# Optimization experiments

Measured on AMD Instinct MI355X. Metric: run time of the kernel, lower is better.

The kernel has to match this reference:

```python
import jax, jax.numpy as jnp
import numpy as np

NM = 50000   # member nodes
NP = 50000   # provider nodes
DM = 96      # member feature dim
DP = 128     # provider feature dim
IN_DIM = 128
HID = 256
LAT = 64
E = 1000000


def _sage_conv(x, src, dst, n, Wl, Wr, b):
    # PyG SAGEConv, mean aggregation: out = lin_l(mean_j x_j) + lin_r(x)
    msg = x[src]                                           # [E2, F]
    agg = jax.ops.segment_sum(msg, dst, num_segments=n)    # [N, F]
    deg = jax.ops.segment_sum(jnp.ones(src.shape[0], x.dtype), dst, num_segments=n)
    agg = agg / jnp.maximum(deg, 1.0)[:, None]
    return agg @ Wl.T + b + x @ Wr.T


def setup_inputs() -> dict:
    key = jax.random.key(0)
    ks = jax.random.split(key, 12)
    def g(k, shape, scale):
        return jax.random.normal(k, shape, jnp.float32) * scale
    inp = {
        "x_member": jax.random.normal(ks[0], (NM, DM), jnp.float32),
        "x_provider": jax.random.normal(ks[1], (NP, DP), jnp.float32),
        "edge_index": jnp.stack([
            jax.random.randint(ks[2], (E,), 0, NP),   # provider idx
            jax.random.randint(ks[3], (E,), 0, NM),   # member idx
        ], axis=0),
        # SAGEConv 1
        "W1l": g(ks[4], (HID, IN_DIM), (1.0 / IN_DIM) ** 0.5),
        "W1r": g(ks[5], (HID, IN_DIM), (1.0 / IN_DIM) ** 0.5),
        "b1": jnp.zeros((HID,), jnp.float32),
        # SAGEConv 2
        "W2l": g(ks[6], (LAT, HID), (1.0 / HID) ** 0.5),
        "W2r": g(ks[7], (LAT, HID), (1.0 / HID) ** 0.5),
        "b2": jnp.zeros((LAT,), jnp.float32),
        # decoder Linear(latent, in_dim)
        "Wd": g(ks[8], (IN_DIM, LAT), (1.0 / LAT) ** 0.5),
        "bd": jnp.zeros((IN_DIM,), jnp.float32),
    }
    return inp


def reference(x_member, x_provider, edge_index, W1l, W1r, b1, W2l, W2r, b2, Wd, bd):
    # pad member features to max_dim and concat (members first)
    xm = jnp.pad(x_member, ((0, 0), (0, IN_DIM - DM)))
    x = jnp.concatenate([xm, x_provider], axis=0)          # [NM+NP, IN_DIM]

    provider_idx = edge_index[0]
    member_idx = edge_index[1]
    # faithful to source: member indices are offset by NM in the combined graph
    src = jnp.concatenate([provider_idx, member_idx + NM])
    dst = jnp.concatenate([member_idx + NM, provider_idx])
    n = NM + NP

    h = jax.nn.relu(_sage_conv(x, src, dst, n, W1l, W1r, b1))
    # dropout: eval mode -> identity
    z = _sage_conv(h, src, dst, n, W2l, W2r, b2)            # [N, LAT]
    x_hat = z @ Wd.T + bd                                   # [N, IN_DIM]

    x_hat_member = x_hat[:NM]
    x_hat_provider = x_hat[NM:]
    member_z = z[:NM]
    provider_z = z[NM:]
    edge_logits = jnp.sum(provider_z[provider_idx] * member_z[member_idx], axis=1)
    return (x_hat_member, x_hat_provider, edge_logits)
```

## Files before the change

kernel.cpp:

```cpp
#include <hip/hip_runtime.h>
#include <stdint.h>

#define NMEM 50000
#define NTOT 100000
#define DMEM 96
#define DPRV 128
#define IND  128
#define HID  256
#define LATD 64
#define NEDGE 1000000

#define NB   196
#define VSH  9
#define NBV  512
#define EPB  4096

#define PREP_PCOUNT 245
#define PREP_CANON  418
#define G3B 1563

typedef __bf16 v8bf  __attribute__((ext_vector_type(8)));
typedef float  f32x4 __attribute__((ext_vector_type(4)));

__device__ __forceinline__ float bf2f(uint32_t u) {
    union { uint32_t u; float f; } x; x.u = u << 16; return x.f;
}
__device__ __forceinline__ uint32_t f2bf(float f) {
    union { float f; uint32_t u; } x; x.f = f;
    uint32_t r = x.u + 0x7fffu + ((x.u >> 16) & 1u);
    return r >> 16;
}
__device__ __forceinline__ int ld_ei(const int* ei, int idx, int i64) {
    return i64 ? ei[2 * idx] : ei[idx];
}

__global__ void k_detect(const uint16_t* __restrict__ w1l, const int* __restrict__ ei,
                         int* __restrict__ flags) {
    __shared__ int c1, c2;
    if (threadIdx.x == 0) { c1 = 0; c2 = 0; }
    __syncthreads();
    int big = 0;
    for (int i = threadIdx.x; i < 32768; i += 256) {
        float w = bf2f(w1l[i]);
        if (!(w > -2.0f && w < 2.0f)) big++;
    }
    int zhi = 0;
    for (int j = threadIdx.x; j < 2048; j += 256)
        if (ei[2 * j + 1] == 0) zhi++;
    atomicAdd(&c1, big);
    atomicAdd(&c2, zhi);
    __syncthreads();
    if (threadIdx.x == 0) {
        flags[0] = (c1 > 64) ? 1 : 0;
        flags[1] = (c2 > 1024) ? 1 : 0;
    }
}

__global__ __launch_bounds__(256) void k_prep(const void* w1l, const void* w1r,
                                              const void* w2l, const void* w2r,
                                              const void* wd, const void* b1,
                                              const void* b2, const void* bd,
                                              const void* xm, const void* xp,
                                              const int* __restrict__ ei,
                                              uint16_t* __restrict__ dstw,
                                              float* __restrict__ dstb,
                                              uint16_t* __restrict__ Px,
                                              uint16_t* __restrict__ Rx,
                                              int* __restrict__ bcount,
                                              const int* __restrict__ flags) {
    __shared__ int h[NB];
    int bid = blockIdx.x;
    int t = threadIdx.x;
    int f32in = flags[0];
    if (bid < PREP_PCOUNT) {
        for (int i = t; i < NB; i += 256) h[i] = 0;
        __syncthreads();
        int i64 = flags[1];
        int j0 = bid * EPB;
        int jend = min(j0 + EPB, NEDGE);
        for (int j = j0 + t; j < jend; j += 256) {
            int p = ld_ei(ei, j, i64), m = ld_ei(ei, NEDGE + j, i64);
            atomicAdd(&h[(NMEM + m) >> VSH], 1);
            atomicAdd(&h[p >> VSH], 1);
        }
        __syncthreads();
        for (int i = t; i < NB; i += 256) atomicAdd(&bcount[i], h[i]);
        return;
    }
    if (bid < PREP_PCOUNT + PREP_CANON) {
        int g = (bid - PREP_PCOUNT) * 256 + t;
        if (g < 106496) {
            const void* src; int off;
            if (g < 65536) { int n = g >> 8, k = g & 255;
                src = (k < 128) ? w1l : w1r; off = n * 128 + (k & 127); }
            else if (g < 81920) { src = w2l; off = g - 65536; }
            else if (g < 98304) { src = w2r; off = g - 81920; }
            else                { src = wd;  off = g - 98304; }
            dstw[g] = f32in ? (uint16_t)f2bf(((const float*)src)[off])
                            : ((const uint16_t*)src)[off];
        } else if (g < 106944) {
            int o = g - 106496;
            const void* src; int off;
            if (o < 256)      { src = b1; off = o; }
            else if (o < 320) { src = b2; off = o - 256; }
            else              { src = bd; off = o - 320; }
            dstb[o] = f32in ? ((const float*)src)[off] : bf2f(((const uint16_t*)src)[off]);
        }
        return;
    }
    int idx = (bid - PREP_PCOUNT - PREP_CANON) * 256 + t;
    if (idx >= NTOT * 16) return;
    int v = idx >> 4, dblk = idx & 15;
    int d0 = dblk * 8;
    union { uint4 q; uint16_t u[8]; } o;
    if (v < NMEM) {
        if (d0 < DMEM) {
            if (f32in) {
                const float* s = (const float*)xm + (size_t)v * DMEM + d0;
                uint4 lo = *(const uint4*)s;
                uint4 hi = *(const uint4*)(s + 4);
                const float* lf = (const float*)&lo;
                const float* hf = (const float*)&hi;
#pragma unroll
                for (int i = 0; i < 4; i++) o.u[i] = (uint16_t)f2bf(lf[i]);
#pragma unroll
                for (int i = 0; i < 4; i++) o.u[4 + i] = (uint16_t)f2bf(hf[i]);
            } else {
                o.q = *(const uint4*)((const uint16_t*)xm + (size_t)v * DMEM + d0);
            }
        } else {
            o.q = (uint4){0, 0, 0, 0};
        }
    } else {
        int vv = v - NMEM;
        if (f32in) {
            const float* s = (const float*)xp + (size_t)vv * DPRV + d0;
            uint4 lo = *(const uint4*)s;
            uint4 hi = *(const uint4*)(s + 4);
            const float* lf = (const float*)&lo;
            const float* hf = (const float*)&hi;
#pragma unroll
            for (int i = 0; i < 4; i++) o.u[i] = (uint16_t)f2bf(lf[i]);
#pragma unroll
            for (int i = 0; i < 4; i++) o.u[4 + i] = (uint16_t)f2bf(hf[i]);
        } else {
            o.q = *(const uint4*)((const uint16_t*)xp + (size_t)vv * DPRV + d0);
        }
    }
    if (d0 < 64) *(uint4*)(Px + (size_t)v * 64 + d0) = o.q;
    else         *(uint4*)(Rx + (size_t)v * 64 + (d0 - 64)) = o.q;
}

__global__ void k_bscan(const int* __restrict__ bcount, int* __restrict__ bbase,
                        int* __restrict__ bcursor, int* __restrict__ row_start) {
    __shared__ int s[256];
    int t = threadIdx.x;
    int v = (t < NB) ? bcount[t] : 0;
    s[t] = v; __syncthreads();
    for (int off = 1; off < 256; off <<= 1) {
        int x = (t >= off) ? s[t - off] : 0;
        __syncthreads();
        s[t] += x;
        __syncthreads();
    }
    if (t < NB) { bbase[t] = s[t] - v; bcursor[t] = s[t] - v; }
    if (t == 0) { bbase[NB] = 2 * NEDGE; row_start[NTOT] = 2 * NEDGE; }
}

__global__ __launch_bounds__(256) void k_part(const int* __restrict__ ei,
                                              int* __restrict__ bcursor,
                                              uint32_t* __restrict__ part,
                                              const int* __restrict__ flags) {
    __shared__ int h[NB], gb[NB], cur[NB];
    int t = threadIdx.x;
    for (int i = t; i < NB; i += 256) { h[i] = 0; cur[i] = 0; }
    __syncthreads();
    int i64 = flags[1];
    int j0 = blockIdx.x * EPB;
    int jend = min(j0 + EPB, NEDGE);
    for (int j = j0 + t; j < jend; j += 256) {
        int p = ld_ei(ei, j, i64), m = ld_ei(ei, NEDGE + j, i64);
        atomicAdd(&h[(NMEM + m) >> VSH], 1);
        atomicAdd(&h[p >> VSH], 1);
    }
    __syncthreads();
    for (int i = t; i < NB; i += 256) gb[i] = atomicAdd(&bcursor[i], h[i]);
    __syncthreads();
    for (int j = j0 + t; j < jend; j += 256) {
        int p = ld_ei(ei, j, i64), m = ld_ei(ei, NEDGE + j, i64);
        int d1 = NMEM + m;
        int d2 = p;
        int b1 = d1 >> VSH, b2 = d2 >> VSH;
        int r1 = atomicAdd(&cur[b1], 1);
        part[gb[b1] + r1] = ((uint32_t)(d1 & (NBV - 1)) << 17) | (uint32_t)p;
        int r2 = atomicAdd(&cur[b2], 1);
        part[gb[b2] + r2] = ((uint32_t)(d2 & (NBV - 1)) << 17) | (uint32_t)(NMEM + m);
    }
}

__global__ __launch_bounds__(256) void k_sort(const uint32_t* __restrict__ part,
                                              const int* __restrict__ bbase,
                                              int* __restrict__ row_start,
                                              int* __restrict__ colg) {
    __shared__ int sa[NBV], sb[NBV];
    int k = blockIdx.x, t = threadIdx.x;
    int base = bbase[k];
    int cnt  = bbase[k + 1] - base;
    for (int i = t; i < NBV; i += 256) sa[i] = 0;
    __syncthreads();
    for (int i = t; i < cnt; i += 256) {
        uint32_t e = part[base + i];
        atomicAdd(&sa[e >> 17], 1);
    }
    __syncthreads();
    int* src = sa; int* dst = sb;
    for (int off = 1; off < NBV; off <<= 1) {
        for (int i = t; i < NBV; i += 256)
            dst[i] = src[i] + (i >= off ? src[i - off] : 0);
        __syncthreads();
        int* tmp = src; src = dst; dst = tmp;
    }
    for (int i = t; i < NBV; i += 256) {
        int excl = (i > 0) ? src[i - 1] : 0;
        dst[i] = excl;
        int gv = (k << VSH) + i;
        if (gv < NTOT) row_start[gv] = base + excl;
    }
    __syncthreads();
    for (int i = t; i < cnt; i += 256) {
        uint32_t e = part[base + i];
        int dloc = (int)(e >> 17);
        int pos = atomicAdd(&dst[dloc], 1);
        colg[base + pos] = (int)(e & 0x1FFFFu);
    }
}

__global__ __launch_bounds__(256) void k_agg1(const uint16_t* __restrict__ Px,
                                              const uint16_t* __restrict__ Rx,
                                              const int* __restrict__ row_start,
                                              const int* __restrict__ colg,
                                              uint16_t* __restrict__ A1) {
    int t = threadIdx.x;
    int half = (t & 63) >> 5;
    int v = blockIdx.x * 8 + (t >> 6) * 2 + half;
    int l32 = t & 31;
    int slot = l32 >> 4, cg = l32 & 15;
    const uint16_t* base = (cg < 8) ? Px : Rx;
    int co = (cg & 7) * 8;
    int start = row_start[v], end = row_start[v + 1];
    float a0[8] = {0.f, 0.f, 0.f, 0.f, 0.f, 0.f, 0.f, 0.f};
    float a1[8] = {0.f, 0.f, 0.f, 0.f, 0.f, 0.f, 0.f, 0.f};
    bool skip = (v >= NMEM) && (cg >= 12);
    if (!skip) {
        int b = start + slot;
        for (; b + 2 < end; b += 4) {
            int s0 = colg[b], s1 = colg[b + 2];
            union { uint4 q; uint16_t u[8]; } f0, f1;
            f0.q = *(const uint4*)(base + (size_t)s0 * 64 + co);
            f1.q = *(const uint4*)(base + (size_t)s1 * 64 + co);
#pragma unroll
            for (int i = 0; i < 8; i++) { a0[i] += bf2f(f0.u[i]); a1[i] += bf2f(f1.u[i]); }
        }
        if (b < end) {
            int s0 = colg[b];
            union { uint4 q; uint16_t u[8]; } f0;
            f0.q = *(const uint4*)(base + (size_t)s0 * 64 + co);
#pragma unroll
            for (int i = 0; i < 8; i++) a0[i] += bf2f(f0.u[i]);
        }
    }
#pragma unroll
    for (int i = 0; i < 8; i++) {
        a0[i] += a1[i];
        a0[i] += __shfl_xor(a0[i], 16);
    }
    if (slot == 0) {
        float inv = 1.0f / (float)max(end - start, 1);
        union { uint4 q; uint16_t u[8]; } o;
#pragma unroll
        for (int i = 0; i < 8; i++) o.u[i] = (uint16_t)f2bf(a0[i] * inv);
        *(uint4*)(A1 + (size_t)v * 128 + cg * 8) = o.q;
    }
}

__global__ __launch_bounds__(256, 4) void k_gemm1(const uint16_t* __restrict__ A1,
                                                  const uint16_t* __restrict__ canonb,
                                                  const float* __restrict__ biasf,
                                                  uint16_t* __restrict__ P,
                                                  uint16_t* __restrict__ R) {
    __shared__ uint16_t As[64][264];
    int t = threadIdx.x;
    int w = t >> 6, lane = t & 63;
    int m16 = lane & 15, q = lane >> 4;
    int row0 = blockIdx.x * 64;

    uint4 stg[8];
#pragma unroll
    for (int i = 0; i < 8; i++) {
        int c = t + i * 256;
        int row = c >> 5, seg = c & 31;
        int grow = min(row0 + row, NTOT - 1);
        int k0 = seg * 8;
        const uint16_t* src;
        if (k0 < 128)      src = A1 + (size_t)grow * 128 + k0;
        else if (k0 < 192) src = P + (size_t)grow * 64 + (k0 - 128);
        else               src = R + (size_t)grow * 64 + (k0 - 192);
        stg[i] = *(const uint4*)src;
    }
#pragma unroll
    for (int i = 0; i < 8; i++) {
        int c = t + i * 256;
        *(uint4*)&As[c >> 5][(c & 31) * 8] = stg[i];
    }
    __syncthreads();

    uint32_t hpk[4][4][2];
#pragma unroll
    for (int pn = 0; pn < 4; pn++) {
        int col = w * 64 + pn * 16 + m16;
        v8bf b1[8];
#pragma unroll
        for (int ks = 0; ks < 8; ks++)
            b1[ks] = *(const v8bf*)(canonb + (size_t)col * 256 + ks * 32 + q * 8);
        f32x4 acc[4];
#pragma unroll
        for (int mt = 0; mt < 4; mt++) acc[mt] = (f32x4){0.f, 0.f, 0.f, 0.f};
#pragma unroll
        for (int mt = 0; mt < 4; mt++) {
#pragma unroll
            for (int ks = 0; ks < 8; ks++) {
                v8bf a = *(const v8bf*)&As[mt * 16 + m16][ks * 32 + q * 8];
                acc[mt] = __builtin_amdgcn_mfma_f32_16x16x32_bf16(b1[ks], a, acc[mt], 0, 0, 0);
            }
        }
        int cb = w * 64 + pn * 16 + q * 4;
        f32x4 bb = *(const f32x4*)&biasf[cb];
#pragma unroll
        for (int mt = 0; mt < 4; mt++) {
            float v0 = fmaxf(acc[mt][0] + bb[0], 0.f);
            float v1 = fmaxf(acc[mt][1] + bb[1], 0.f);
            float v2 = fmaxf(acc[mt][2] + bb[2], 0.f);
            float v3 = fmaxf(acc[mt][3] + bb[3], 0.f);
            hpk[pn][mt][0] = f2bf(v0) | (f2bf(v1) << 16);
            hpk[pn][mt][1] = f2bf(v2) | (f2bf(v3) << 16);
        }
        __builtin_amdgcn_sched_barrier(0);
    }
    __syncthreads();

#pragma unroll
    for (int pn = 0; pn < 4; pn++) {
        int cb = w * 64 + pn * 16 + q * 4;
#pragma unroll
        for (int mt = 0; mt < 4; mt++) {
            uint2 v; v.x = hpk[pn][mt][0]; v.y = hpk[pn][mt][1];
            *(uint2*)&As[mt * 16 + m16][cb] = v;
        }
    }
    __syncthreads();

    v8bf b2[2][8];
#pragma unroll
    for (int n = 0; n < 2; n++) {
        int c2 = w * 32 + n * 16 + m16;
        const uint16_t* s2 = canonb + (c2 < 64 ? (65536 + c2 * 256) : (81920 + (c2 - 64) * 256));
#pragma unroll
        for (int ks = 0; ks < 8; ks++)
            b2[n][ks] = *(const v8bf*)(s2 + ks * 32 + q * 8);
    }
    f32x4 acc2[4][2];
#pragma unroll
    for (int mt = 0; mt < 4; mt++) {
        acc2[mt][0] = (f32x4){0.f, 0.f, 0.f, 0.f};
        acc2[mt][1] = (f32x4){0.f, 0.f, 0.f, 0.f};
    }
#pragma unroll
    for (int mt = 0; mt < 4; mt++) {
#pragma unroll
        for (int ks = 0; ks < 8; ks++) {
            v8bf hf = *(const v8bf*)&As[mt * 16 + m16][ks * 32 + q * 8];
            acc2[mt][0] = __builtin_amdgcn_mfma_f32_16x16x32_bf16(b2[0][ks], hf, acc2[mt][0], 0, 0, 0);
            acc2[mt][1] = __builtin_amdgcn_mfma_f32_16x16x32_bf16(b2[1][ks], hf, acc2[mt][1], 0, 0, 0);
        }
    }
#pragma unroll
    for (int n = 0; n < 2; n++) {
        int cb = w * 32 + n * 16 + q * 4;
        int isR = cb >= 64;
        int cl = cb - (isR ? 64 : 0);
        f32x4 bb;
        if (isR) bb = *(const f32x4*)&biasf[256 + cl];
        else     bb = (f32x4){0.f, 0.f, 0.f, 0.f};
        uint16_t* dst = isR ? R : P;
#pragma unroll
        for (int mt = 0; mt < 4; mt++) {
            int row = row0 + mt * 16 + m16;
            if (row < NTOT) {
                uint2 v;
                v.x = f2bf(acc2[mt][n][0] + bb[0]) | (f2bf(acc2[mt][n][1] + bb[1]) << 16);
                v.y = f2bf(acc2[mt][n][2] + bb[2]) | (f2bf(acc2[mt][n][3] + bb[3]) << 16);
                *(uint2*)(dst + (size_t)row * 64 + cl) = v;
            }
        }
    }
}

__global__ __launch_bounds__(256) void k_agg2z(const uint16_t* __restrict__ P,
                                               const uint16_t* __restrict__ R,
                                               const int* __restrict__ row_start,
                                               const int* __restrict__ colg,
                                               uint16_t* __restrict__ Z) {
    int t = threadIdx.x;
    int half = (t & 63) >> 5;
    int v = blockIdx.x * 8 + (t >> 6) * 2 + half;
    int l32 = t & 31;
    int slot = l32 >> 3, cg = l32 & 7;
    int start = row_start[v], end = row_start[v + 1];
    float a0[8] = {0.f, 0.f, 0.f, 0.f, 0.f, 0.f, 0.f, 0.f};
    float a1[8] = {0.f, 0.f, 0.f, 0.f, 0.f, 0.f, 0.f, 0.f};
    int b = start + slot;
    for (; b + 4 < end; b += 8) {
        int s0 = colg[b], s1 = colg[b + 4];
        union { uint4 q; uint16_t u[8]; } f0, f1;
        f0.q = *(const uint4*)(P + (size_t)s0 * 64 + cg * 8);
        f1.q = *(const uint4*)(P + (size_t)s1 * 64 + cg * 8);
#pragma unroll
        for (int i = 0; i < 8; i++) { a0[i] += bf2f(f0.u[i]); a1[i] += bf2f(f1.u[i]); }
    }
    if (b < end) {
        int s0 = colg[b];
        union { uint4 q; uint16_t u[8]; } f0;
        f0.q = *(const uint4*)(P + (size_t)s0 * 64 + cg * 8);
#pragma unroll
        for (int i = 0; i < 8; i++) a0[i] += bf2f(f0.u[i]);
    }
#pragma unroll
    for (int i = 0; i < 8; i++) {
        a0[i] += a1[i];
        a0[i] += __shfl_xor(a0[i], 8);
        a0[i] += __shfl_xor(a0[i], 16);
    }
    if (slot == 0) {
        float inv = 1.0f / (float)max(end - start, 1);
        union { uint4 q; uint16_t u[8]; } rr, o;
        rr.q = *(const uint4*)(R + (size_t)v * 64 + cg * 8);
#pragma unroll
        for (int i = 0; i < 8; i++)
            o.u[i] = (uint16_t)f2bf(a0[i] * inv + bf2f(rr.u[i]));
        *(uint4*)(Z + (size_t)v * 64 + cg * 8) = o.q;
    }
}

__global__ __launch_bounds__(256, 4) void k_out(const int* __restrict__ ei,
                                                const uint16_t* __restrict__ Z,
                                                const uint16_t* __restrict__ canonb,
                                                const float* __restrict__ biasf,
                                                float* __restrict__ outf,
                                                const int* __restrict__ flags) {
    int bid = blockIdx.x;
    if (bid < G3B) {
        int wave = threadIdx.x >> 6, lane = threadIdx.x & 63;
        int m16 = lane & 15, quad = lane >> 4;
        int row0 = (bid * 4 + wave) * 16;
        int arow = min(row0 + m16, NTOT - 1);
        v8bf a0 = *(const v8bf*)(Z + (size_t)arow * 64 + quad * 8);
        v8bf a1 = *(const v8bf*)(Z + (size_t)arow * 64 + 32 + quad * 8);
        v8bf b0[8], b1[8];
#pragma unroll
        for (int nt = 0; nt < 8; nt++) {
            b0[nt] = *(const v8bf*)(canonb + 98304 + (size_t)(nt * 16 + m16) * 64 + quad * 8);
            b1[nt] = *(const v8bf*)(canonb + 98304 + (size_t)(nt * 16 + m16) * 64 + 32 + quad * 8);
        }
        f32x4 acc[8];
#pragma unroll
        for (int i = 0; i < 8; i++) acc[i] = (f32x4){0.f, 0.f, 0.f, 0.f};
#pragma unroll
        for (int nt = 0; nt < 8; nt++) {
            acc[nt] = __builtin_amdgcn_mfma_f32_16x16x32_bf16(a0, b0[nt], acc[nt], 0, 0, 0);
            acc[nt] = __builtin_amdgcn_mfma_f32_16x16x32_bf16(a1, b1[nt], acc[nt], 0, 0, 0);
        }
#pragma unroll
        for (int nt = 0; nt < 8; nt++) {
            int col = nt * 16 + m16;
            float bia = biasf[320 + col];
#pragma unroll
            for (int r = 0; r < 4; r++) {
                int row = row0 + quad * 4 + r;
                if (row < NTOT) outf[(size_t)row * 128 + col] = acc[nt][r] + bia;
            }
        }
        return;
    }
    int t = (bid - G3B) * 256 + threadIdx.x;
    int j = t >> 3, sub = t & 7;
    if (j >= NEDGE) return;
    int i64 = flags[1];
    int p = ld_ei(ei, j, i64), m = ld_ei(ei, NEDGE + j, i64);
    union { uint4 q; uint16_t u[8]; } a, b;
    a.q = *(const uint4*)(Z + (size_t)(NMEM + p) * 64 + sub * 8);
    b.q = *(const uint4*)(Z + (size_t)m * 64 + sub * 8);
    float d = 0.f;
#pragma unroll
    for (int i = 0; i < 8; i++) d += bf2f(a.u[i]) * bf2f(b.u[i]);
    d += __shfl_xor(d, 1);
    d += __shfl_xor(d, 2);
    d += __shfl_xor(d, 4);
    if (sub == 0) outf[12800000 + j] = d;
}

__global__ void k_zero_out(float* __restrict__ out, int n4) {
    int i = blockIdx.x * 256 + threadIdx.x;
    if (i < n4) ((uint4*)out)[i] = (uint4){0, 0, 0, 0};
}
__global__ void k_sentinel(float* __restrict__ out, const int* __restrict__ flags,
                           int ws_mb) {
    if (blockIdx.x == 0 && threadIdx.x == 0)
        out[0] = 1000.0f + (float)ws_mb + 4096.0f * flags[0] + 8192.0f * flags[1];
}

extern "C" void kernel_launch(void* const* d_in, const int* in_sizes, int n_in,
                              void* d_out, int out_size, void* d_ws, size_t ws_size,
                              hipStream_t stream) {
    const void* xm = d_in[0];
    const void* xp = d_in[1];
    const int*  ei = (const int*)d_in[2];
    float* outf = (float*)d_out;

    const size_t NEED = 73019648;
    if (ws_size < NEED) {
        int* flags = (int*)d_ws;
        k_detect<<<1, 256, 0, stream>>>((const uint16_t*)d_in[3], ei, flags);
        int n4 = out_size / 4;
        k_zero_out<<<(n4 + 255) / 256, 256, 0, stream>>>(outf, n4);
        k_sentinel<<<1, 64, 0, stream>>>(outf, flags, (int)(ws_size >> 20));
        return;
    }

    char* ws = (char*)d_ws;
    int* colg       = (int*)(ws + 0);
    int* bmeta      = (int*)(ws + 8000000);
    int* bucket_count  = bmeta;
    int* bucket_base   = bmeta + 256;
    int* bucket_cursor = bmeta + 512;
    int* row_start  = (int*)(ws + 8400384);
    int* flags      = (int*)(ws + 8800768) + 100;
    uint16_t* canonb= (uint16_t*)(ws + 8804864);
    float* biasf    = (float*)(ws + 9017856);
    uint16_t* A1    = (uint16_t*)(ws + 9019648);
    uint32_t* part  = (uint32_t*)A1;
    uint16_t* P     = (uint16_t*)(ws + 34619648);
    uint16_t* R     = (uint16_t*)(ws + 47419648);
    uint16_t* Z     = (uint16_t*)(ws + 60219648);

    k_detect<<<1, 256, 0, stream>>>((const uint16_t*)d_in[3], ei, flags);
    hipMemsetAsync(bucket_count, 0, 256 * sizeof(int), stream);
    k_prep<<<PREP_PCOUNT + PREP_CANON + (NTOT * 16 + 255) / 256, 256, 0, stream>>>(
        d_in[3], d_in[4], d_in[6], d_in[7], d_in[9], d_in[5], d_in[8], d_in[10],
        xm, xp, ei, canonb, biasf, P, R, bucket_count, flags);
    k_bscan<<<1, 256, 0, stream>>>(bucket_count, bucket_base, bucket_cursor, row_start);
    k_part<<<PREP_PCOUNT, 256, 0, stream>>>(ei, bucket_cursor, part, flags);
    k_sort<<<NB, 256, 0, stream>>>(part, bucket_base, row_start, colg);
    k_agg1<<<NTOT / 8, 256, 0, stream>>>(P, R, row_start, colg, A1);
    k_gemm1<<<(NTOT + 63) / 64, 256, 0, stream>>>(A1, canonb, biasf, P, R);
    k_agg2z<<<NTOT / 8, 256, 0, stream>>>(P, R, row_start, colg, Z);
    k_out<<<G3B + NEDGE * 8 / 256, 256, 0, stream>>>(ei, Z, canonb, biasf, outf, flags);
}
```

Before: 391.4 us.

## Store gathered node features and layer-2 projections in FP8 to cut gather bandwidth

The prep kernel now also writes an FP8 (e4m3) copy of each node's 128-dim input features. The first aggregation gathers those 8-byte chunks instead of bf16 16-byte chunks. The first GEMM now writes the projection P in FP8, and the second aggregation gathers it from there, which halves the bytes moved in both random-access gather passes. Buffers are reassigned: Z reuses the A1 region, and X8/P8 share one region. The cost is reduced precision in the mean aggregations, which may exceed output tolerance. The member-row padding skip in agg1 is also dropped, so every node now loads all 128 columns.

```diff
diff --git a/kernel.cpp b/kernel.cpp
--- a/kernel.cpp
+++ b/kernel.cpp
@@ -21,6 +21,7 @@
 
 typedef __bf16 v8bf  __attribute__((ext_vector_type(8)));
 typedef float  f32x4 __attribute__((ext_vector_type(4)));
+typedef float  f32x2 __attribute__((ext_vector_type(2)));
 
 __device__ __forceinline__ float bf2f(uint32_t u) {
     union { uint32_t u; float f; } x; x.u = u << 16; return x.f;
@@ -32,6 +33,16 @@
 }
 __device__ __forceinline__ int ld_ei(const int* ei, int idx, int i64) {
     return i64 ? ei[2 * idx] : ei[idx];
+}
+__device__ __forceinline__ uint32_t fp8pk4(float f0, float f1, float f2, float f3) {
+    uint32_t w = __builtin_amdgcn_cvt_pk_fp8_f32(f0, f1, 0, false);
+    w = __builtin_amdgcn_cvt_pk_fp8_f32(f2, f3, w, true);
+    return w;
+}
+__device__ __forceinline__ void fp8x4_acc(uint32_t w, float* a) {
+    f32x2 lo = __builtin_amdgcn_cvt_pk_f32_fp8(w, false);
+    f32x2 hi = __builtin_amdgcn_cvt_pk_f32_fp8(w, true);
+    a[0] += lo.x; a[1] += lo.y; a[2] += hi.x; a[3] += hi.y;
 }
 
 __global__ void k_detect(const uint16_t* __restrict__ w1l, const int* __restrict__ ei,
@@ -66,6 +77,7 @@
                                               float* __restrict__ dstb,
                                               uint16_t* __restrict__ Px,
                                               uint16_t* __restrict__ Rx,
+                                              uint8_t* __restrict__ X8,
                                               int* __restrict__ bcount,
                                               const int* __restrict__ flags) {
     __shared__ int h[NB];
@@ -149,6 +161,10 @@
     }
     if (d0 < 64) *(uint4*)(Px + (size_t)v * 64 + d0) = o.q;
     else         *(uint4*)(Rx + (size_t)v * 64 + (d0 - 64)) = o.q;
+    uint2 x8;
+    x8.x = fp8pk4(bf2f(o.u[0]), bf2f(o.u[1]), bf2f(o.u[2]), bf2f(o.u[3]));
+    x8.y = fp8pk4(bf2f(o.u[4]), bf2f(o.u[5]), bf2f(o.u[6]), bf2f(o.u[7]));
+    *(uint2*)(X8 + (size_t)v * 128 + d0) = x8;
 }
 
 __global__ void k_bscan(const int* __restrict__ bcount, int* __restrict__ bbase,
@@ -235,8 +251,7 @@
     }
 }
 
-__global__ __launch_bounds__(256) void k_agg1(const uint16_t* __restrict__ Px,
-                                              const uint16_t* __restrict__ Rx,
+__global__ __launch_bounds__(256) void k_agg1(const uint8_t* __restrict__ X8,
                                               const int* __restrict__ row_start,
                                               const int* __restrict__ colg,
                                               uint16_t* __restrict__ A1) {
@@ -245,29 +260,21 @@
     int v = blockIdx.x * 8 + (t >> 6) * 2 + half;
     int l32 = t & 31;
     int slot = l32 >> 4, cg = l32 & 15;
-    const uint16_t* base = (cg < 8) ? Px : Rx;
-    int co = (cg & 7) * 8;
     int start = row_start[v], end = row_start[v + 1];
     float a0[8] = {0.f, 0.f, 0.f, 0.f, 0.f, 0.f, 0.f, 0.f};
     float a1[8] = {0.f, 0.f, 0.f, 0.f, 0.f, 0.f, 0.f, 0.f};
-    bool skip = (v >= NMEM) && (cg >= 12);
-    if (!skip) {
-        int b = start + slot;
-        for (; b + 2 < end; b += 4) {
-            int s0 = colg[b], s1 = colg[b + 2];
-            union { uint4 q; uint16_t u[8]; } f0, f1;
-            f0.q = *(const uint4*)(base + (size_t)s0 * 64 + co);
-            f1.q = *(const uint4*)(base + (size_t)s1 * 64 + co);
-#pragma unroll
-            for (int i = 0; i < 8; i++) { a0[i] += bf2f(f0.u[i]); a1[i] += bf2f(f1.u[i]); }
-        }
-        if (b < end) {
-            int s0 = colg[b];
-            union { uint4 q; uint16_t u[8]; } f0;
-            f0.q = *(const uint4*)(base + (size_t)s0 * 64 + co);
-#pragma unroll
-            for (int i = 0; i < 8; i++) a0[i] += bf2f(f0.u[i]);
-        }
+    int b = start + slot;
+    for (; b + 2 < end; b += 4) {
+        int s0 = colg[b], s1 = colg[b + 2];
+        uint2 g0 = *(const uint2*)(X8 + (size_t)s0 * 128 + cg * 8);
+        uint2 g1 = *(const uint2*)(X8 + (size_t)s1 * 128 + cg * 8);
+        fp8x4_acc(g0.x, a0); fp8x4_acc(g0.y, a0 + 4);
+        fp8x4_acc(g1.x, a1); fp8x4_acc(g1.y, a1 + 4);
+    }
+    if (b < end) {
+        int s0 = colg[b];
+        uint2 g0 = *(const uint2*)(X8 + (size_t)s0 * 128 + cg * 8);
+        fp8x4_acc(g0.x, a0); fp8x4_acc(g0.y, a0 + 4);
     }
 #pragma unroll
     for (int i = 0; i < 8; i++) {
@@ -286,8 +293,9 @@
 __global__ __launch_bounds__(256, 4) void k_gemm1(const uint16_t* __restrict__ A1,
                                                   const uint16_t* __restrict__ canonb,
                                                   const float* __restrict__ biasf,
-                                                  uint16_t* __restrict__ P,
-                                                  uint16_t* __restrict__ R) {
+                                                  const uint16_t* __restrict__ Px,
+                                                  uint16_t* __restrict__ Rx,
+                                                  uint8_t* __restrict__ P8) {
     __shared__ uint16_t As[64][264];
     int t = threadIdx.x;
     int w = t >> 6, lane = t & 63;
@@ -303,8 +311,8 @@
         int k0 = seg * 8;
         const uint16_t* src;
         if (k0 < 128)      src = A1 + (size_t)grow * 128 + k0;
-        else if (k0 < 192) src = P + (size_t)grow * 64 + (k0 - 128);
-        else               src = R + (size_t)grow * 64 + (k0 - 192);
+        else if (k0 < 192) src = Px + (size_t)grow * 64 + (k0 - 128);
+        else               src = Rx + (size_t)grow * 64 + (k0 - 192);
         stg[i] = *(const uint4*)src;
     }
 #pragma unroll
@@ -388,24 +396,33 @@
         int cb = w * 32 + n * 16 + q * 4;
         int isR = cb >= 64;
         int cl = cb - (isR ? 64 : 0);
-        f32x4 bb;
-        if (isR) bb = *(const f32x4*)&biasf[256 + cl];
-        else     bb = (f32x4){0.f, 0.f, 0.f, 0.f};
-        uint16_t* dst = isR ? R : P;
-#pragma unroll
-        for (int mt = 0; mt < 4; mt++) {
-            int row = row0 + mt * 16 + m16;
-            if (row < NTOT) {
-                uint2 v;
-                v.x = f2bf(acc2[mt][n][0] + bb[0]) | (f2bf(acc2[mt][n][1] + bb[1]) << 16);
-                v.y = f2bf(acc2[mt][n][2] + bb[2]) | (f2bf(acc2[mt][n][3] + bb[3]) << 16);
-                *(uint2*)(dst + (size_t)row * 64 + cl) = v;
+        if (isR) {
+            f32x4 bb = *(const f32x4*)&biasf[256 + cl];
+#pragma unroll
+            for (int mt = 0; mt < 4; mt++) {
+                int row = row0 + mt * 16 + m16;
+                if (row < NTOT) {
+                    uint2 v;
+                    v.x = f2bf(acc2[mt][n][0] + bb[0]) | (f2bf(acc2[mt][n][1] + bb[1]) << 16);
+                    v.y = f2bf(acc2[mt][n][2] + bb[2]) | (f2bf(acc2[mt][n][3] + bb[3]) << 16);
+                    *(uint2*)(Rx + (size_t)row * 64 + cl) = v;
+                }
             }
-        }
-    }
-}
-
-__global__ __launch_bounds__(256) void k_agg2z(const uint16_t* __restrict__ P,
+        } else {
+#pragma unroll
+            for (int mt = 0; mt < 4; mt++) {
+                int row = row0 + mt * 16 + m16;
+                if (row < NTOT) {
+                    uint32_t pw = fp8pk4(acc2[mt][n][0], acc2[mt][n][1],
+                                         acc2[mt][n][2], acc2[mt][n][3]);
+                    *(uint32_t*)(P8 + (size_t)row * 64 + cl) = pw;
+                }
+            }
+        }
+    }
+}
+
+__global__ __launch_bounds__(256) void k_agg2z(const uint8_t* __restrict__ P8,
                                                const uint16_t* __restrict__ R,
                                                const int* __restrict__ row_start,
                                                const int* __restrict__ colg,
@@ -421,18 +438,15 @@
     int b = start + slot;
     for (; b + 4 < end; b += 8) {
         int s0 = colg[b], s1 = colg[b + 4];
-        union { uint4 q; uint16_t u[8]; } f0, f1;
-        f0.q = *(const uint4*)(P + (size_t)s0 * 64 + cg * 8);
-        f1.q = *(const uint4*)(P + (size_t)s1 * 64 + cg * 8);
-#pragma unroll
-        for (int i = 0; i < 8; i++) { a0[i] += bf2f(f0.u[i]); a1[i] += bf2f(f1.u[i]); }
+        uint2 g0 = *(const uint2*)(P8 + (size_t)s0 * 64 + cg * 8);
+        uint2 g1 = *(const uint2*)(P8 + (size_t)s1 * 64 + cg * 8);
+        fp8x4_acc(g0.x, a0); fp8x4_acc(g0.y, a0 + 4);
+        fp8x4_acc(g1.x, a1); fp8x4_acc(g1.y, a1 + 4);
     }
     if (b < end) {
         int s0 = colg[b];
-        union { uint4 q; uint16_t u[8]; } f0;
-        f0.q = *(const uint4*)(P + (size_t)s0 * 64 + cg * 8);
-#pragma unroll
-        for (int i = 0; i < 8; i++) a0[i] += bf2f(f0.u[i]);
+        uint2 g0 = *(const uint2*)(P8 + (size_t)s0 * 64 + cg * 8);
+        fp8x4_acc(g0.x, a0); fp8x4_acc(g0.y, a0 + 4);
     }
 #pragma unroll
     for (int i = 0; i < 8; i++) {
@@ -548,20 +562,22 @@
     float* biasf    = (float*)(ws + 9017856);
     uint16_t* A1    = (uint16_t*)(ws + 9019648);
     uint32_t* part  = (uint32_t*)A1;
-    uint16_t* P     = (uint16_t*)(ws + 34619648);
-    uint16_t* R     = (uint16_t*)(ws + 47419648);
-    uint16_t* Z     = (uint16_t*)(ws + 60219648);
+    uint16_t* Zn    = (uint16_t*)(ws + 9019648);
+    uint16_t* Px    = (uint16_t*)(ws + 34619648);
+    uint16_t* Rx    = (uint16_t*)(ws + 47419648);
+    uint8_t*  X8    = (uint8_t*)(ws + 60219648);
+    uint8_t*  P8    = (uint8_t*)(ws + 60219648);
 
     k_detect<<<1, 256, 0, stream>>>((const uint16_t*)d_in[3], ei, flags);
     hipMemsetAsync(bucket_count, 0, 256 * sizeof(int), stream);
     k_prep<<<PREP_PCOUNT + PREP_CANON + (NTOT * 16 + 255) / 256, 256, 0, stream>>>(
         d_in[3], d_in[4], d_in[6], d_in[7], d_in[9], d_in[5], d_in[8], d_in[10],
-        xm, xp, ei, canonb, biasf, P, R, bucket_count, flags);
+        xm, xp, ei, canonb, biasf, Px, Rx, X8, bucket_count, flags);
     k_bscan<<<1, 256, 0, stream>>>(bucket_count, bucket_base, bucket_cursor, row_start);
     k_part<<<PREP_PCOUNT, 256, 0, stream>>>(ei, bucket_cursor, part, flags);
     k_sort<<<NB, 256, 0, stream>>>(part, bucket_base, row_start, colg);
-    k_agg1<<<NTOT / 8, 256, 0, stream>>>(P, R, row_start, colg, A1);
-    k_gemm1<<<(NTOT + 63) / 64, 256, 0, stream>>>(A1, canonb, biasf, P, R);
-    k_agg2z<<<NTOT / 8, 256, 0, stream>>>(P, R, row_start, colg, Z);
-    k_out<<<G3B + NEDGE * 8 / 256, 256, 0, stream>>>(ei, Z, canonb, biasf, outf, flags);
-}
+    k_agg1<<<NTOT / 8, 256, 0, stream>>>(X8, row_start, colg, A1);
+    k_gemm1<<<(NTOT + 63) / 64, 256, 0, stream>>>(A1, canonb, biasf, Px, Rx, P8);
+    k_agg2z<<<NTOT / 8, 256, 0, stream>>>(P8, Rx, row_start, colg, Zn);
+    k_out<<<G3B + NEDGE * 8 / 256, 256, 0, stream>>>(ei, Zn, canonb, biasf, outf, flags);
+}
```

Measured after the change: 373.1 us. -4.7%, faster.
